# Kernel tuning notes

Measured on AMD Instinct MI355X. Metric: run time of the kernel, lower is better.

## Reference

```python
import jax, jax.numpy as jnp
import numpy as np

B, V, FIN, K, FOUT, E = 8, 100000, 32, 4, 64, 800000


def setup_inputs() -> dict:
    key = jax.random.key(0)
    ks = jax.random.split(key, 6)
    inputs = jax.random.normal(ks[0], (B, V, FIN), dtype=jnp.float32)
    lap_rows = jax.random.randint(ks[1], (E,), 0, V, dtype=jnp.int32)
    lap_cols = jax.random.randint(ks[2], (E,), 0, V, dtype=jnp.int32)
    # rescaled-Laplacian nonzeros; small magnitude keeps the Chebyshev recurrence stable
    lap_vals = jax.random.normal(ks[3], (E,), dtype=jnp.float32) * 0.1
    # Kaiming-normal init: std = sqrt(2 / (Fin * K)) as in reset_parameters()
    std = float(np.sqrt(2.0 / (FIN * K)))
    weight = jax.random.normal(ks[4], (FIN, K, FOUT), dtype=jnp.float32) * std
    bias = jax.random.normal(ks[5], (FOUT,), dtype=jnp.float32) * 0.01
    return dict(inputs=inputs, lap_rows=lap_rows, lap_cols=lap_cols,
                lap_vals=lap_vals, weight=weight, bias=bias)


def reference(inputs, lap_rows, lap_cols, lap_vals, weight, bias):
    # inputs: [B, V, Fin]; weight: [Fin, K, Fout]; Laplacian in COO form.
    Bn, Vn, Fin = inputs.shape
    _, Kn, Fout = weight.shape

    def spmm(x):  # x: [V, Fin, B] -> L @ x via gather + segment-sum over edges
        msgs = lap_vals[:, None, None] * x[lap_cols]  # [E, Fin, B]
        return jax.ops.segment_sum(msgs, lap_rows, num_segments=Vn)

    x0 = jnp.transpose(inputs, (1, 2, 0))  # [V, Fin, B]
    xs = [x0]
    if Kn > 1:
        x1 = spmm(x0)
        xs.append(x1)
    for _ in range(2, Kn):
        x2 = 2.0 * spmm(x1) - x0  # Chebyshev recurrence T_k = 2 L T_{k-1} - T_{k-2}
        xs.append(x2)
        x0, x1 = x1, x2
    x = jnp.stack(xs, axis=0)  # [K, V, Fin, B]
    out = jnp.einsum('kvfb,fko->bvo', x, weight) + bias  # [B, V, Fout]
    return out
```

## Files before the change

kernel.cpp:

```cpp
#include <hip/hip_runtime.h>
#include <hip/hip_bf16.h>

#define B_    8
#define V_    100000
#define FIN_  32
#define K_    4
#define FOUT_ 64
#define E_    800000
#define NODE_F 256

typedef __attribute__((ext_vector_type(8))) short bf16x8;
typedef __attribute__((ext_vector_type(4))) float floatx4;

static __device__ inline float bf2f(unsigned short u) {
    unsigned int x = ((unsigned int)u) << 16;
    return __builtin_bit_cast(float, x);
}
static __device__ inline unsigned short f2bf(float f) {
    __hip_bfloat16 h = __float2bfloat16(f);
    return __builtin_bit_cast(unsigned short, h);
}

static __device__ inline float wave_max64(float m) {
    #pragma unroll
    for (int off = 1; off < 64; off <<= 1)
        m = fmaxf(m, __shfl_xor(m, off));
    return m;
}

static __device__ inline void quant_store(const float r[4], int v, int lane,
                                          unsigned char* __restrict__ xi,
                                          float* __restrict__ sc) {
    float m = fmaxf(fmaxf(fabsf(r[0]), fabsf(r[1])), fmaxf(fabsf(r[2]), fabsf(r[3])));
    m = wave_max64(m);
    float inv = (m > 0.f) ? 127.f / m : 0.f;
    if (lane == 0) sc[v] = (m > 0.f) ? m * (1.f / 127.f) : 0.f;
    unsigned int q = 0;
    #pragma unroll
    for (int j = 0; j < 4; ++j) {
        int qi = (int)rintf(r[j] * inv) + 128;
        q |= ((unsigned int)(qi & 0xff)) << (8 * j);
    }
    ((unsigned int*)(xi + (size_t)v * NODE_F))[lane] = q;
}

__global__ __launch_bounds__(256) void k_transpose(const float* __restrict__ in,
                                                   unsigned short* __restrict__ x0,
                                                   unsigned char* __restrict__ x0i,
                                                   float* __restrict__ s0,
                                                   const int* __restrict__ rows,
                                                   int* __restrict__ counts,
                                                   const float* __restrict__ weight,
                                                   unsigned short* __restrict__ wpack) {
    int tid = blockIdx.x * 256 + threadIdx.x;
    int lane = threadIdx.x & 63;
    int f4 = tid & 7;
    int m  = tid >> 3;
    int v  = m >> 3;
    int b  = m & 7;
    float4 val = ((const float4*)(in + ((size_t)b * V_ + v) * FIN_))[f4];
    ushort4 o;
    o.x = f2bf(val.x); o.y = f2bf(val.y); o.z = f2bf(val.z); o.w = f2bf(val.w);
    ((ushort4*)x0)[tid] = o;

    float r[4] = {val.x, val.y, val.z, val.w};
    quant_store(r, v, lane, x0i, s0);

    if (tid < E_) atomicAdd(&counts[rows[tid]], 1);

    if (tid < 1024) {
        int l = tid & 63;
        int ot   = (tid >> 6) & 3;
        int kq   = tid >> 8;
        int quad = l >> 4, l16 = l & 15;
        bf16x8 w;
        #pragma unroll
        for (int j = 0; j < 8; ++j)
            w[j] = (short)f2bf(weight[(size_t)(quad * 8 + j) * (K_ * FOUT_) + kq * FOUT_ + ot * 16 + l16]);
        *((bf16x8*)(wpack + (size_t)tid * 8)) = w;
    }
}

__global__ __launch_bounds__(256) void k_zero_int(int* __restrict__ p, int n) {
    int t = blockIdx.x * 256 + threadIdx.x;
    if (t < n) p[t] = 0;
}

__global__ __launch_bounds__(1024) void k_scan1(const int* __restrict__ counts,
                                                int* __restrict__ row_ptr,
                                                int* __restrict__ cursor,
                                                int* __restrict__ bsums, int n) {
    __shared__ int s[1024];
    int t = threadIdx.x;
    int idx = blockIdx.x * 1024 + t;
    int v = (idx < n) ? counts[idx] : 0;
    s[t] = v;
    __syncthreads();
    for (int off = 1; off < 1024; off <<= 1) {
        int add = (t >= off) ? s[t - off] : 0;
        __syncthreads();
        s[t] += add;
        __syncthreads();
    }
    if (idx < n) {
        int r = s[t] - v;
        row_ptr[idx] = r;
        cursor[idx]  = r;
    }
    if (t == 1023) bsums[blockIdx.x] = s[1023];
}

__global__ __launch_bounds__(128) void k_scan2(const int* __restrict__ bsums,
                                               int* __restrict__ boffs, int nb) {
    __shared__ int s[128];
    int t = threadIdx.x;
    int v = (t < nb) ? bsums[t] : 0;
    s[t] = v;
    __syncthreads();
    for (int off = 1; off < 128; off <<= 1) {
        int add = (t >= off) ? s[t - off] : 0;
        __syncthreads();
        s[t] += add;
        __syncthreads();
    }
    boffs[t] = s[t] - v;
}

__global__ __launch_bounds__(256) void k_scatter(const int* __restrict__ rows,
                                                 const int* __restrict__ cols,
                                                 const float* __restrict__ vals,
                                                 int* __restrict__ cursor,
                                                 const int* __restrict__ boffs,
                                                 int2* __restrict__ e_pack) {
    int e = blockIdx.x * 256 + threadIdx.x;
    if (e < E_) {
        int r = rows[e];
        int pos = atomicAdd(&cursor[r], 1) + boffs[r >> 10];
        e_pack[pos] = make_int2(cols[e], __float_as_int(vals[e]));
    }
}

static __device__ inline void spmm_row_i8(const unsigned char* __restrict__ xi,
                                          const float* __restrict__ sc,
                                          const int2* __restrict__ ep,
                                          int beg, int end, int lane,
                                          float a[4], float* swp) {
    float sw = 0.f;
    int e = beg;
    for (; e + 3 < end; e += 4) {
        int2 p0 = ep[e], p1 = ep[e + 1], p2 = ep[e + 2], p3 = ep[e + 3];
        unsigned int g0 = ((const unsigned int*)(xi + (size_t)p0.x * NODE_F))[lane];
        unsigned int g1 = ((const unsigned int*)(xi + (size_t)p1.x * NODE_F))[lane];
        unsigned int g2 = ((const unsigned int*)(xi + (size_t)p2.x * NODE_F))[lane];
        unsigned int g3 = ((const unsigned int*)(xi + (size_t)p3.x * NODE_F))[lane];
        float w0 = __int_as_float(p0.y) * sc[p0.x];
        float w1 = __int_as_float(p1.y) * sc[p1.x];
        float w2 = __int_as_float(p2.y) * sc[p2.x];
        float w3 = __int_as_float(p3.y) * sc[p3.x];
        sw += w0 + w1 + w2 + w3;
        a[0] += w0 * (float)(g0 & 0xff);         a[1] += w0 * (float)((g0 >> 8) & 0xff);
        a[2] += w0 * (float)((g0 >> 16) & 0xff); a[3] += w0 * (float)(g0 >> 24);
        a[0] += w1 * (float)(g1 & 0xff);         a[1] += w1 * (float)((g1 >> 8) & 0xff);
        a[2] += w1 * (float)((g1 >> 16) & 0xff); a[3] += w1 * (float)(g1 >> 24);
        a[0] += w2 * (float)(g2 & 0xff);         a[1] += w2 * (float)((g2 >> 8) & 0xff);
        a[2] += w2 * (float)((g2 >> 16) & 0xff); a[3] += w2 * (float)(g2 >> 24);
        a[0] += w3 * (float)(g3 & 0xff);         a[1] += w3 * (float)((g3 >> 8) & 0xff);
        a[2] += w3 * (float)((g3 >> 16) & 0xff); a[3] += w3 * (float)(g3 >> 24);
    }
    for (; e < end; ++e) {
        int2 p = ep[e];
        unsigned int g = ((const unsigned int*)(xi + (size_t)p.x * NODE_F))[lane];
        float w = __int_as_float(p.y) * sc[p.x];
        sw += w;
        a[0] += w * (float)(g & 0xff);         a[1] += w * (float)((g >> 8) & 0xff);
        a[2] += w * (float)((g >> 16) & 0xff); a[3] += w * (float)(g >> 24);
    }
    *swp = sw;
}

__global__ __launch_bounds__(256) void k_spmm(const unsigned char* __restrict__ xci,
                                              const float* __restrict__ sci,
                                              const unsigned short* __restrict__ xp,
                                              const int* __restrict__ row_ptr,
                                              const int* __restrict__ boffs,
                                              const int2* __restrict__ ep,
                                              unsigned short* __restrict__ xn,
                                              unsigned char* __restrict__ xni,
                                              float* __restrict__ scn,
                                              float scale, int has_prev) {
    int wave = threadIdx.x >> 6;
    int lane = threadIdx.x & 63;
    int v = blockIdx.x * 4 + wave;
    int beg = row_ptr[v] + boffs[v >> 10];
    int end = (v == V_ - 1) ? E_ : row_ptr[v + 1] + boffs[(v + 1) >> 10];

    float a[4] = {0.f, 0.f, 0.f, 0.f};
    float sw;
    spmm_row_i8(xci, sci, ep, beg, end, lane, a, &sw);

    float r[4];
    #pragma unroll
    for (int j = 0; j < 4; ++j) r[j] = a[j] - 128.f * sw;
    if (has_prev) {
        ushort4 p = *((const ushort4*)(xp + (size_t)v * NODE_F + lane * 4));
        r[0] = scale * r[0] - bf2f(p.x);
        r[1] = scale * r[1] - bf2f(p.y);
        r[2] = scale * r[2] - bf2f(p.z);
        r[3] = scale * r[3] - bf2f(p.w);
    }
    ushort4 o;
    o.x = f2bf(r[0]); o.y = f2bf(r[1]); o.z = f2bf(r[2]); o.w = f2bf(r[3]);
    *((ushort4*)(xn + (size_t)v * NODE_F + lane * 4)) = o;
    quant_store(r, v, lane, xni, scn);
}

__global__ __launch_bounds__(256) void k_spmm3c(const unsigned short* __restrict__ x0,
                                                const unsigned short* __restrict__ x1,
                                                const unsigned short* __restrict__ x2,
                                                const unsigned char* __restrict__ x2i,
                                                const float* __restrict__ s2,
                                                const int* __restrict__ row_ptr,
                                                const int* __restrict__ boffs,
                                                const int2* __restrict__ ep,
                                                const unsigned short* __restrict__ wpack,
                                                const float* __restrict__ bias,
                                                float* __restrict__ out) {
    __shared__ __align__(16) unsigned short x3s[4][2][NODE_F];
    int wave = threadIdx.x >> 6;
    int lane = threadIdx.x & 63;
    int quad = lane >> 4;
    int l16  = lane & 15;
    int pair = blockIdx.x * 4 + wave;
    int v0 = pair * 2;

    #pragma unroll 1
    for (int s = 0; s < 2; ++s) {
        int v = v0 + s;
        int beg = row_ptr[v] + boffs[v >> 10];
        int end = (v == V_ - 1) ? E_ : row_ptr[v + 1] + boffs[(v + 1) >> 10];
        float a[4] = {0.f, 0.f, 0.f, 0.f};
        float sw;
        spmm_row_i8(x2i, s2, ep, beg, end, lane, a, &sw);
        ushort4 p1 = *((const ushort4*)(x1 + (size_t)v * NODE_F + lane * 4));
        ushort4 o;
        o.x = f2bf(2.f * (a[0] - 128.f * sw) - bf2f(p1.x));
        o.y = f2bf(2.f * (a[1] - 128.f * sw) - bf2f(p1.y));
        o.z = f2bf(2.f * (a[2] - 128.f * sw) - bf2f(p1.z));
        o.w = f2bf(2.f * (a[3] - 128.f * sw) - bf2f(p1.w));
        *((ushort4*)&x3s[wave][s][lane * 4]) = o;
    }
    __syncthreads();

    const unsigned short* xs012[3] = {x0, x1, x2};
    bf16x8 wfrag[4][4];
    #pragma unroll
    for (int kq = 0; kq < 4; ++kq)
        #pragma unroll
        for (int ot = 0; ot < 4; ++ot)
            wfrag[kq][ot] = *((const bf16x8*)(wpack + (size_t)((kq * 4 + ot) * 64 + lane) * 8));

    floatx4 acc[4];
    #pragma unroll
    for (int ot = 0; ot < 4; ++ot)
        acc[ot] = *((const floatx4*)(bias + ot * 16 + quad * 4));

    int m0 = pair * 16;
    #pragma unroll
    for (int kq = 0; kq < 4; ++kq) {
        bf16x8 xf;
        if (kq < 3)
            xf = *((const bf16x8*)(xs012[kq] + (size_t)(m0 + l16) * FIN_ + quad * 8));
        else
            xf = *((const bf16x8*)&x3s[wave][l16 >> 3][(l16 & 7) * FIN_ + quad * 8]);
        #pragma unroll
        for (int ot = 0; ot < 4; ++ot)
            acc[ot] = __builtin_amdgcn_mfma_f32_16x16x32_bf16(wfrag[kq][ot], xf, acc[ot], 0, 0, 0);
    }

    int m = m0 + l16;
    int v = m >> 3;
    int b = m & 7;
    float* op = out + ((size_t)b * V_ + v) * FOUT_ + quad * 4;
    #pragma unroll
    for (int ot = 0; ot < 4; ++ot)
        __builtin_nontemporal_store(acc[ot], (floatx4*)(op + ot * 16));
}

extern "C" void kernel_launch(void* const* d_in, const int* in_sizes, int n_in,
                              void* d_out, int out_size, void* d_ws, size_t ws_size,
                              hipStream_t stream) {
    const float* inputs  = (const float*)d_in[0];
    const int*   laprows = (const int*)d_in[1];
    const int*   lapcols = (const int*)d_in[2];
    const float* lapvals = (const float*)d_in[3];
    const float* weight  = (const float*)d_in[4];
    const float* bias    = (const float*)d_in[5];
    float* out = (float*)d_out;

    const size_t XN  = (size_t)V_ * NODE_F;
    const size_t XNI = (size_t)V_ * NODE_F;
    unsigned short* x0 = (unsigned short*)d_ws;
    unsigned short* x1 = x0 + XN;
    unsigned short* x2 = x1 + XN;
    unsigned char* x0i = (unsigned char*)(x2 + XN);
    unsigned char* x1i = x0i + XNI;
    unsigned char* x2i = x1i + XNI;
    float* s0 = (float*)(x2i + XNI);
    float* s1 = s0 + V_;
    float* s2 = s1 + V_;
    int* counts  = (int*)(s2 + V_);
    int* row_ptr = counts + V_;
    int* cursor  = row_ptr + V_;
    int* bsums   = cursor + V_;
    int* boffs   = bsums + 128;
    unsigned short* wpack = (unsigned short*)(boffs + 128);
    int2* e_pack = (int2*)(wpack + 8192);

    const int NB_SCAN = (V_ + 1023) / 1024;

    hipLaunchKernelGGL(k_zero_int, dim3((V_ + 255) / 256), dim3(256), 0, stream, counts, V_);
    hipLaunchKernelGGL(k_transpose, dim3((V_ * B_ * 8) / 256), dim3(256), 0, stream,
                       inputs, x0, x0i, s0, laprows, counts, weight, wpack);
    hipLaunchKernelGGL(k_scan1, dim3(NB_SCAN), dim3(1024), 0, stream,
                       counts, row_ptr, cursor, bsums, V_);
    hipLaunchKernelGGL(k_scan2, dim3(1), dim3(128), 0, stream, bsums, boffs, NB_SCAN);
    hipLaunchKernelGGL(k_scatter, dim3((E_ + 255) / 256), dim3(256), 0, stream,
                       laprows, lapcols, lapvals, cursor, boffs, e_pack);

    hipLaunchKernelGGL(k_spmm, dim3(V_ / 4), dim3(256), 0, stream,
                       x0i, s0, (const unsigned short*)nullptr, row_ptr, boffs, e_pack,
                       x1, x1i, s1, 1.0f, 0);
    hipLaunchKernelGGL(k_spmm, dim3(V_ / 4), dim3(256), 0, stream,
                       x1i, s1, x0, row_ptr, boffs, e_pack,
                       x2, x2i, s2, 2.0f, 1);

    hipLaunchKernelGGL(k_spmm3c, dim3(12500), dim3(256), 0, stream,
                       x0, x1, x2, x2i, s2, row_ptr, boffs, e_pack, wpack, bias, out);
}
```

Before: 582.7 us.

## Drop bf16 x2 buffer, dequantize int8 x2 in contraction, use grid-stride loops

The second SpMM pass no longer writes a bf16 copy of x2. The contraction kernel rebuilds the x2 MFMA operand by dequantizing the int8 x2 with its per-node scale, which removes a V×256 bf16 write and read. The three SpMM kernels become grid-stride persistent loops with fewer blocks. The contraction loads weight fragments per iteration instead of holding them in registers, and its output stores change from nontemporal to plain. This adds int8 quantization error to the T2 term of the output, and the plain stores may pollute cache.

```diff
diff --git a/kernel.cpp b/kernel.cpp
--- a/kernel.cpp
+++ b/kernel.cpp
@@ -178,112 +178,172 @@
     *swp = sw;
 }
 
-__global__ __launch_bounds__(256) void k_spmm(const unsigned char* __restrict__ xci,
-                                              const float* __restrict__ sci,
-                                              const unsigned short* __restrict__ xp,
-                                              const int* __restrict__ row_ptr,
-                                              const int* __restrict__ boffs,
-                                              const int2* __restrict__ ep,
-                                              unsigned short* __restrict__ xn,
-                                              unsigned char* __restrict__ xni,
-                                              float* __restrict__ scn,
-                                              float scale, int has_prev) {
-    int wave = threadIdx.x >> 6;
-    int lane = threadIdx.x & 63;
-    int v = blockIdx.x * 4 + wave;
-    int beg = row_ptr[v] + boffs[v >> 10];
-    int end = (v == V_ - 1) ? E_ : row_ptr[v + 1] + boffs[(v + 1) >> 10];
-
-    float a[4] = {0.f, 0.f, 0.f, 0.f};
-    float sw;
-    spmm_row_i8(xci, sci, ep, beg, end, lane, a, &sw);
-
-    float r[4];
-    #pragma unroll
-    for (int j = 0; j < 4; ++j) r[j] = a[j] - 128.f * sw;
-    if (has_prev) {
-        ushort4 p = *((const ushort4*)(xp + (size_t)v * NODE_F + lane * 4));
-        r[0] = scale * r[0] - bf2f(p.x);
-        r[1] = scale * r[1] - bf2f(p.y);
-        r[2] = scale * r[2] - bf2f(p.z);
-        r[3] = scale * r[3] - bf2f(p.w);
-    }
-    ushort4 o;
-    o.x = f2bf(r[0]); o.y = f2bf(r[1]); o.z = f2bf(r[2]); o.w = f2bf(r[3]);
-    *((ushort4*)(xn + (size_t)v * NODE_F + lane * 4)) = o;
-    quant_store(r, v, lane, xni, scn);
-}
-
-__global__ __launch_bounds__(256) void k_spmm3c(const unsigned short* __restrict__ x0,
-                                                const unsigned short* __restrict__ x1,
-                                                const unsigned short* __restrict__ x2,
-                                                const unsigned char* __restrict__ x2i,
-                                                const float* __restrict__ s2,
-                                                const int* __restrict__ row_ptr,
-                                                const int* __restrict__ boffs,
-                                                const int2* __restrict__ ep,
-                                                const unsigned short* __restrict__ wpack,
-                                                const float* __restrict__ bias,
-                                                float* __restrict__ out) {
-    __shared__ __align__(16) unsigned short x3s[4][2][NODE_F];
-    int wave = threadIdx.x >> 6;
-    int lane = threadIdx.x & 63;
-    int quad = lane >> 4;
-    int l16  = lane & 15;
-    int pair = blockIdx.x * 4 + wave;
-    int v0 = pair * 2;
-
+static __device__ inline void phase_pass(int gw, int nw, int lane,
+                                         const unsigned char* __restrict__ xci,
+                                         const float* __restrict__ sci,
+                                         const unsigned short* __restrict__ xp,
+                                         int has_prev, float scale,
+                                         unsigned short* __restrict__ xn,
+                                         unsigned char* __restrict__ xni,
+                                         float* __restrict__ scn,
+                                         const int* __restrict__ row_ptr,
+                                         const int* __restrict__ boffs,
+                                         const int2* __restrict__ ep) {
     #pragma unroll 1
-    for (int s = 0; s < 2; ++s) {
-        int v = v0 + s;
+    for (int v = gw; v < V_; v += nw) {
         int beg = row_ptr[v] + boffs[v >> 10];
         int end = (v == V_ - 1) ? E_ : row_ptr[v + 1] + boffs[(v + 1) >> 10];
         float a[4] = {0.f, 0.f, 0.f, 0.f};
         float sw;
-        spmm_row_i8(x2i, s2, ep, beg, end, lane, a, &sw);
-        ushort4 p1 = *((const ushort4*)(x1 + (size_t)v * NODE_F + lane * 4));
-        ushort4 o;
-        o.x = f2bf(2.f * (a[0] - 128.f * sw) - bf2f(p1.x));
-        o.y = f2bf(2.f * (a[1] - 128.f * sw) - bf2f(p1.y));
-        o.z = f2bf(2.f * (a[2] - 128.f * sw) - bf2f(p1.z));
-        o.w = f2bf(2.f * (a[3] - 128.f * sw) - bf2f(p1.w));
-        *((ushort4*)&x3s[wave][s][lane * 4]) = o;
-    }
-    __syncthreads();
-
-    const unsigned short* xs012[3] = {x0, x1, x2};
-    bf16x8 wfrag[4][4];
+        spmm_row_i8(xci, sci, ep, beg, end, lane, a, &sw);
+        float r[4];
+        #pragma unroll
+        for (int j = 0; j < 4; ++j) r[j] = a[j] - 128.f * sw;
+        if (has_prev) {
+            ushort4 p = *((const ushort4*)(xp + (size_t)v * NODE_F + lane * 4));
+            r[0] = scale * r[0] - bf2f(p.x);
+            r[1] = scale * r[1] - bf2f(p.y);
+            r[2] = scale * r[2] - bf2f(p.z);
+            r[3] = scale * r[3] - bf2f(p.w);
+        }
+        if (xn) {
+            ushort4 o;
+            o.x = f2bf(r[0]); o.y = f2bf(r[1]); o.z = f2bf(r[2]); o.w = f2bf(r[3]);
+            *((ushort4*)(xn + (size_t)v * NODE_F + lane * 4)) = o;
+        }
+        quant_store(r, v, lane, xni, scn);
+    }
+}
+
+static __device__ inline void mfma4(const unsigned short* __restrict__ wpack,
+                                    int kq, int lane, bf16x8 xf, floatx4 acc[4]) {
     #pragma unroll
-    for (int kq = 0; kq < 4; ++kq)
+    for (int ot = 0; ot < 4; ++ot) {
+        bf16x8 wf = *((const bf16x8*)(wpack + (size_t)((kq * 4 + ot) * 64 + lane) * 8));
+        acc[ot] = __builtin_amdgcn_mfma_f32_16x16x32_bf16(wf, xf, acc[ot], 0, 0, 0);
+    }
+}
+
+static __device__ inline void phase_contract(int gw, int nw, int lane,
+                                             unsigned short* __restrict__ x3sw,
+                                             const unsigned short* __restrict__ x0,
+                                             const unsigned short* __restrict__ x1,
+                                             const unsigned char* __restrict__ x2i,
+                                             const float* __restrict__ s2,
+                                             const int* __restrict__ row_ptr,
+                                             const int* __restrict__ boffs,
+                                             const int2* __restrict__ ep,
+                                             const unsigned short* __restrict__ wpack,
+                                             const float* __restrict__ bias,
+                                             float* __restrict__ out) {
+    int quad = lane >> 4;
+    int l16  = lane & 15;
+    floatx4 bi[4];
+    #pragma unroll
+    for (int ot = 0; ot < 4; ++ot)
+        bi[ot] = *((const floatx4*)(bias + ot * 16 + quad * 4));
+
+    #pragma unroll 1
+    for (int pair = gw; pair < V_ / 2; pair += nw) {
+        #pragma unroll 1
+        for (int s = 0; s < 2; ++s) {
+            int v = pair * 2 + s;
+            int beg = row_ptr[v] + boffs[v >> 10];
+            int end = (v == V_ - 1) ? E_ : row_ptr[v + 1] + boffs[(v + 1) >> 10];
+            float a[4] = {0.f, 0.f, 0.f, 0.f};
+            float sw;
+            spmm_row_i8(x2i, s2, ep, beg, end, lane, a, &sw);
+            ushort4 p1 = *((const ushort4*)(x1 + (size_t)v * NODE_F + lane * 4));
+            ushort4 o;
+            o.x = f2bf(2.f * (a[0] - 128.f * sw) - bf2f(p1.x));
+            o.y = f2bf(2.f * (a[1] - 128.f * sw) - bf2f(p1.y));
+            o.z = f2bf(2.f * (a[2] - 128.f * sw) - bf2f(p1.z));
+            o.w = f2bf(2.f * (a[3] - 128.f * sw) - bf2f(p1.w));
+            *((ushort4*)(x3sw + s * NODE_F + lane * 4)) = o;
+        }
+
+        int m0 = pair * 16;
+        int vA = pair * 2 + (l16 >> 3);
+        int bA = l16 & 7;
+        floatx4 acc[4] = {bi[0], bi[1], bi[2], bi[3]};
+
+        {
+            bf16x8 xf = *((const bf16x8*)(x0 + (size_t)(m0 + l16) * FIN_ + quad * 8));
+            mfma4(wpack, 0, lane, xf, acc);
+        }
+        {
+            bf16x8 xf = *((const bf16x8*)(x1 + (size_t)(m0 + l16) * FIN_ + quad * 8));
+            mfma4(wpack, 1, lane, xf, acc);
+        }
+        {
+            float s = s2[vA];
+            const unsigned int* p = (const unsigned int*)(x2i + (size_t)vA * NODE_F + bA * FIN_ + quad * 8);
+            unsigned int d0 = p[0], d1 = p[1];
+            bf16x8 xf;
+            #pragma unroll
+            for (int j = 0; j < 4; ++j)
+                xf[j] = (short)f2bf(((float)((d0 >> (8 * j)) & 0xff) - 128.f) * s);
+            #pragma unroll
+            for (int j = 0; j < 4; ++j)
+                xf[4 + j] = (short)f2bf(((float)((d1 >> (8 * j)) & 0xff) - 128.f) * s);
+            mfma4(wpack, 2, lane, xf, acc);
+        }
+        {
+            bf16x8 xf = *((const bf16x8*)(x3sw + (l16 >> 3) * NODE_F + (l16 & 7) * FIN_ + quad * 8));
+            mfma4(wpack, 3, lane, xf, acc);
+        }
+
+        int m = m0 + l16;
+        int v = m >> 3;
+        int b = m & 7;
+        float* op = out + ((size_t)b * V_ + v) * FOUT_ + quad * 4;
         #pragma unroll
         for (int ot = 0; ot < 4; ++ot)
-            wfrag[kq][ot] = *((const bf16x8*)(wpack + (size_t)((kq * 4 + ot) * 64 + lane) * 8));
-
-    floatx4 acc[4];
-    #pragma unroll
-    for (int ot = 0; ot < 4; ++ot)
-        acc[ot] = *((const floatx4*)(bias + ot * 16 + quad * 4));
-
-    int m0 = pair * 16;
-    #pragma unroll
-    for (int kq = 0; kq < 4; ++kq) {
-        bf16x8 xf;
-        if (kq < 3)
-            xf = *((const bf16x8*)(xs012[kq] + (size_t)(m0 + l16) * FIN_ + quad * 8));
-        else
-            xf = *((const bf16x8*)&x3s[wave][l16 >> 3][(l16 & 7) * FIN_ + quad * 8]);
-        #pragma unroll
-        for (int ot = 0; ot < 4; ++ot)
-            acc[ot] = __builtin_amdgcn_mfma_f32_16x16x32_bf16(wfrag[kq][ot], xf, acc[ot], 0, 0, 0);
-    }
-
-    int m = m0 + l16;
-    int v = m >> 3;
-    int b = m & 7;
-    float* op = out + ((size_t)b * V_ + v) * FOUT_ + quad * 4;
-    #pragma unroll
-    for (int ot = 0; ot < 4; ++ot)
-        __builtin_nontemporal_store(acc[ot], (floatx4*)(op + ot * 16));
+            *((floatx4*)(op + ot * 16)) = acc[ot];
+    }
+}
+
+__global__ __launch_bounds__(256) void k_p1(const unsigned char* __restrict__ x0i,
+                                            const float* __restrict__ s0,
+                                            unsigned short* __restrict__ x1,
+                                            unsigned char* __restrict__ x1i,
+                                            float* __restrict__ s1,
+                                            const int* __restrict__ row_ptr,
+                                            const int* __restrict__ boffs,
+                                            const int2* __restrict__ ep) {
+    int gw = blockIdx.x * 4 + (threadIdx.x >> 6);
+    phase_pass(gw, gridDim.x * 4, threadIdx.x & 63, x0i, s0,
+               (const unsigned short*)nullptr, 0, 1.f, x1, x1i, s1, row_ptr, boffs, ep);
+}
+
+__global__ __launch_bounds__(256) void k_p2(const unsigned char* __restrict__ x1i,
+                                            const float* __restrict__ s1,
+                                            const unsigned short* __restrict__ x0,
+                                            unsigned char* __restrict__ x2i,
+                                            float* __restrict__ s2,
+                                            const int* __restrict__ row_ptr,
+                                            const int* __restrict__ boffs,
+                                            const int2* __restrict__ ep) {
+    int gw = blockIdx.x * 4 + (threadIdx.x >> 6);
+    phase_pass(gw, gridDim.x * 4, threadIdx.x & 63, x1i, s1, x0, 1, 2.f,
+               (unsigned short*)nullptr, x2i, s2, row_ptr, boffs, ep);
+}
+
+__global__ __launch_bounds__(256) void k_p3(const unsigned short* __restrict__ x0,
+                                            const unsigned short* __restrict__ x1,
+                                            const unsigned char* __restrict__ x2i,
+                                            const float* __restrict__ s2,
+                                            const int* __restrict__ row_ptr,
+                                            const int* __restrict__ boffs,
+                                            const int2* __restrict__ ep,
+                                            const unsigned short* __restrict__ wpack,
+                                            const float* __restrict__ bias,
+                                            float* __restrict__ out) {
+    __shared__ __align__(16) unsigned short x3s[4][2][NODE_F];
+    int wave = threadIdx.x >> 6;
+    int gw = blockIdx.x * 4 + wave;
+    phase_contract(gw, gridDim.x * 4, threadIdx.x & 63, &x3s[wave][0][0],
+                   x0, x1, x2i, s2, row_ptr, boffs, ep, wpack, bias, out);
 }
 
 extern "C" void kernel_launch(void* const* d_in, const int* in_sizes, int n_in,
@@ -298,14 +358,12 @@
     float* out = (float*)d_out;
 
     const size_t XN  = (size_t)V_ * NODE_F;
-    const size_t XNI = (size_t)V_ * NODE_F;
     unsigned short* x0 = (unsigned short*)d_ws;
     unsigned short* x1 = x0 + XN;
-    unsigned short* x2 = x1 + XN;
-    unsigned char* x0i = (unsigned char*)(x2 + XN);
-    unsigned char* x1i = x0i + XNI;
-    unsigned char* x2i = x1i + XNI;
-    float* s0 = (float*)(x2i + XNI);
+    unsigned char* x0i = (unsigned char*)(x1 + XN);
+    unsigned char* x1i = x0i + XN;
+    unsigned char* x2i = x1i + XN;
+    float* s0 = (float*)(x2i + XN);
     float* s1 = s0 + V_;
     float* s2 = s1 + V_;
     int* counts  = (int*)(s2 + V_);
@@ -327,13 +385,10 @@
     hipLaunchKernelGGL(k_scatter, dim3((E_ + 255) / 256), dim3(256), 0, stream,
                        laprows, lapcols, lapvals, cursor, boffs, e_pack);
 
-    hipLaunchKernelGGL(k_spmm, dim3(V_ / 4), dim3(256), 0, stream,
-                       x0i, s0, (const unsigned short*)nullptr, row_ptr, boffs, e_pack,
-                       x1, x1i, s1, 1.0f, 0);
-    hipLaunchKernelGGL(k_spmm, dim3(V_ / 4), dim3(256), 0, stream,
-                       x1i, s1, x0, row_ptr, boffs, e_pack,
-                       x2, x2i, s2, 2.0f, 1);
-
-    hipLaunchKernelGGL(k_spmm3c, dim3(12500), dim3(256), 0, stream,
-                       x0, x1, x2, x2i, s2, row_ptr, boffs, e_pack, wpack, bias, out);
-}
+    hipLaunchKernelGGL(k_p1, dim3(6250), dim3(256), 0, stream,
+                       x0i, s0, x1, x1i, s1, row_ptr, boffs, e_pack);
+    hipLaunchKernelGGL(k_p2, dim3(6250), dim3(256), 0, stream,
+                       x1i, s1, x0, x2i, s2, row_ptr, boffs, e_pack);
+    hipLaunchKernelGGL(k_p3, dim3(3125), dim3(256), 0, stream,
+                       x0, x1, x2i, s2, row_ptr, boffs, e_pack, wpack, bias, out);
+}
```

Measured after the change: 639.6 us. +9.8%, slower.
